# Optimization experiments

Hardware: AMD Instinct MI355X
Metric: run time of the kernel (lower is better)

Reference implementation:

```python
import jax, jax.numpy as jnp
import numpy as np

NS, NR, D, H, O = 50000, 100000, 128, 128, 2
ESR, ERR, ESS = 1000000, 1600000, 800000


def _sage(x_src, x_dst, src, dst, Wl, bl, Wr, num_dst):
    # PyG SAGEConv(aggr='mean'): lin_l(mean_{j in N(i)} x_j) + lin_r(x_i)
    s = jax.ops.segment_sum(x_src[src], dst, num_segments=num_dst)
    cnt = jax.ops.segment_sum(jnp.ones(dst.shape, x_src.dtype), dst, num_segments=num_dst)
    agg = s / jnp.maximum(cnt, 1.0)[:, None]
    return agg @ Wl + bl + x_dst @ Wr


def setup_inputs() -> dict:
    key = jax.random.key(0)
    ks = jax.random.split(key, 32)
    f = lambda i, shp: jax.random.normal(ks[i], shp, jnp.float32) * 0.05
    inp = {"x_subject": f(0, (NS, D)), "x_roi": f(1, (NR, D))}
    wnames = ["w1_sr_l", "w1_sr_r", "w1_rr_l", "w1_rr_r", "w1_ss_l", "w1_ss_r",
              "w2_sr_l", "w2_sr_r", "w2_rr_l", "w2_rr_r", "w2_ss_l", "w2_ss_r"]
    for i, n in enumerate(wnames):
        inp[n] = f(2 + i, (D if n[1] == '1' else H, H))
    for n in ["b1_sr", "b1_rr", "b1_ss", "b2_sr", "b2_rr", "b2_ss"]:
        inp[n] = jnp.zeros((H,), jnp.float32)
    inp["lin_w"] = f(14, (H, O))
    inp["lin_b"] = jnp.zeros((O,), jnp.float32)
    inp["ei_sr_src"] = jax.random.randint(ks[20], (ESR,), 0, NS, jnp.int32)
    inp["ei_sr_dst"] = jax.random.randint(ks[21], (ESR,), 0, NR, jnp.int32)
    inp["ei_rr_src"] = jax.random.randint(ks[22], (ERR,), 0, NR, jnp.int32)
    inp["ei_rr_dst"] = jax.random.randint(ks[23], (ERR,), 0, NR, jnp.int32)
    inp["ei_ss_src"] = jax.random.randint(ks[24], (ESS,), 0, NS, jnp.int32)
    inp["ei_ss_dst"] = jax.random.randint(ks[25], (ESS,), 0, NS, jnp.int32)
    return inp


def reference(x_subject, x_roi,
              w1_sr_l, b1_sr, w1_sr_r, w1_rr_l, b1_rr, w1_rr_r, w1_ss_l, b1_ss, w1_ss_r,
              w2_sr_l, b2_sr, w2_sr_r, w2_rr_l, b2_rr, w2_rr_r, w2_ss_l, b2_ss, w2_ss_r,
              lin_w, lin_b,
              ei_sr_src, ei_sr_dst, ei_rr_src, ei_rr_dst, ei_ss_src, ei_ss_dst):
    # layer 1: HeteroConv with aggr='mean' over per-edge-type outputs
    r1 = 0.5 * (_sage(x_subject, x_roi, ei_sr_src, ei_sr_dst, w1_sr_l, b1_sr, w1_sr_r, NR)
                + _sage(x_roi, x_roi, ei_rr_src, ei_rr_dst, w1_rr_l, b1_rr, w1_rr_r, NR))
    s1 = _sage(x_subject, x_subject, ei_ss_src, ei_ss_dst, w1_ss_l, b1_ss, w1_ss_r, NS)
    r1, s1 = jax.nn.relu(r1), jax.nn.relu(s1)
    # layer 2 (roi branch is dead code w.r.t. the output, which reads only 'subject')
    s2 = _sage(s1, s1, ei_ss_src, ei_ss_dst, w2_ss_l, b2_ss, w2_ss_r, NS)
    s2 = jax.nn.relu(s2)
    return s2 @ lin_w + lin_b
```

## Files before the change

### kernel.cpp

```cpp
#include <hip/hip_runtime.h>

#define NS   50000
#define ESS  800000
#define D    128

#define BSPAN 256
#define NB    ((NS + BSPAN - 1) / BSPAN)
#define EPB   4096
#define NBLK  ((ESS + EPB - 1) / EPB)
#define BCAP  8192

#define SPLIT_BLOCKS (NS * D / 8 / 256)
#define PREP_BLOCKS  256

typedef __attribute__((ext_vector_type(8))) short bf16x8;
typedef __attribute__((ext_vector_type(4))) float f32x4;

static __device__ __forceinline__ ushort f2bf(float f) {
    uint u = __float_as_uint(f);
    u += 0x7fffu + ((u >> 16) & 1u);
    return (ushort)(u >> 16);
}
static __device__ __forceinline__ float bf2f(ushort h) {
    return __uint_as_float((uint)h << 16);
}

__global__ __launch_bounds__(256) void splitprep_k(
    const float* __restrict__ x, ushort* __restrict__ xh,
    const float* __restrict__ w1l, const float* __restrict__ w1r,
    const float* __restrict__ w2l, const float* __restrict__ w2r,
    ushort* __restrict__ wt1h, ushort* __restrict__ wt1l,
    ushort* __restrict__ wt2h, ushort* __restrict__ wt2l,
    int* __restrict__ btotal)
{
    int blk = blockIdx.x, t = threadIdx.x;
    if (blk < SPLIT_BLOCKS) {
        int i = blk * 256 + t;
        const float4* src = (const float4*)(x + (size_t)i * 8);
        float4 a = src[0], b = src[1];
        uint4 o;
        o.x = (uint)f2bf(a.x) | ((uint)f2bf(a.y) << 16);
        o.y = (uint)f2bf(a.z) | ((uint)f2bf(a.w) << 16);
        o.z = (uint)f2bf(b.x) | ((uint)f2bf(b.y) << 16);
        o.w = (uint)f2bf(b.z) | ((uint)f2bf(b.w) << 16);
        *(uint4*)(xh + (size_t)i * 8) = o;
    } else if (blk < SPLIT_BLOCKS + PREP_BLOCKS) {
        int g = (blk - SPLIT_BLOCKS) * 256 + t;
        int layer = g >> 15;
        int rem   = g & 32767;
        int k     = rem >> 7;
        int col   = rem & 127;
        const float* wl = layer ? w2l : w1l;
        const float* wr = layer ? w2r : w1r;
        float v = (k < 128) ? wl[k * 128 + col] : wr[(k - 128) * 128 + col];
        ushort h = f2bf(v);
        ushort l = f2bf(v - bf2f(h));
        size_t idx = ((size_t)((k >> 5) * 4 + ((k >> 3) & 3)) * 128 + col) * 8 + (k & 7);
        (layer ? wt2h : wt1h)[idx] = h;
        (layer ? wt2l : wt1l)[idx] = l;
    } else {
        if (t < NB) btotal[t] = 0;
    }
}

__global__ __launch_bounds__(256) void pack_k(
    const int* __restrict__ src, const int* __restrict__ dst,
    uint* __restrict__ staging, int* __restrict__ blockhist,
    int* __restrict__ blockstart, int* __restrict__ btotal)
{
    __shared__ uint ldata[EPB];
    __shared__ int lh[256], lofs[256], lcur[256];
    int t = threadIdx.x, blk = blockIdx.x;
    int base = blk * EPB;
    int nmine = min(EPB, ESS - base);
    lh[t] = 0;
    __syncthreads();
    for (int i = t; i < nmine; i += 256) {
        int s = src[base + i], d = dst[base + i];
        ldata[i] = (uint)s | ((uint)(d & 255) << 16) | ((uint)(d >> 8) << 24);
        atomicAdd(&lh[d >> 8], 1);
    }
    __syncthreads();
    int v = lh[t];
    lofs[t] = v;
    __syncthreads();
    for (int off = 1; off < 256; off <<= 1) {
        int o = (t >= off) ? lofs[t - off] : 0;
        __syncthreads();
        lofs[t] += o;
        __syncthreads();
    }
    int excl = lofs[t] - v;
    if (t < NB) {
        blockhist[blk * NB + t]  = v;
        blockstart[blk * NB + t] = excl;
        if (v) atomicAdd(&btotal[t], v);
    }
    lcur[t] = excl;
    __syncthreads();
    for (int i = t; i < nmine; i += 256) {
        uint p = ldata[i];
        int slot = atomicAdd(&lcur[p >> 24], 1);
        staging[base + slot] = p;
    }
}

__global__ __launch_bounds__(256) void scan196_k(
    const int* __restrict__ btotal, int* __restrict__ bucket_base)
{
    __shared__ int lds[256];
    int t = threadIdx.x;
    int v = (t < NB) ? btotal[t] : 0;
    lds[t] = v;
    __syncthreads();
    for (int off = 1; off < 256; off <<= 1) {
        int o = (t >= off) ? lds[t - off] : 0;
        __syncthreads();
        lds[t] += o;
        __syncthreads();
    }
    if (t < NB) bucket_base[t] = lds[t] - v;
}

__global__ __launch_bounds__(256) void bucket_csr_k(
    const uint* __restrict__ staging, const int* __restrict__ blockhist,
    const int* __restrict__ blockstart, const int* __restrict__ bucket_base,
    int* __restrict__ deg, int* __restrict__ row_start, int* __restrict__ esrc)
{
    __shared__ uint bdata[BCAP];
    __shared__ int lscan[256], ldeg[256], lcur[256];
    int b = blockIdx.x, t = threadIdx.x;
    int c = (t < NBLK) ? blockhist[t * NB + b] : 0;
    lscan[t] = c;
    __syncthreads();
    for (int off = 1; off < 256; off <<= 1) {
        int o = (t >= off) ? lscan[t - off] : 0;
        __syncthreads();
        lscan[t] += o;
        __syncthreads();
    }
    int total = min(lscan[255], BCAP);
    int excl  = lscan[t] - c;
    if (t < NBLK && c > 0) {
        const uint* sp = staging + (size_t)t * EPB + blockstart[t * NB + b];
        for (int i = 0; i < c; ++i)
            if (excl + i < BCAP) bdata[excl + i] = sp[i];
    }
    ldeg[t] = 0;
    __syncthreads();
    for (int i = t; i < total; i += 256)
        atomicAdd(&ldeg[(bdata[i] >> 16) & 255], 1);
    __syncthreads();
    int v = ldeg[t];
    lscan[t] = v;
    __syncthreads();
    for (int off = 1; off < 256; off <<= 1) {
        int o = (t >= off) ? lscan[t - off] : 0;
        __syncthreads();
        lscan[t] += o;
        __syncthreads();
    }
    int nexcl = lscan[t] - v;
    int gbase = bucket_base[b];
    int node  = b * BSPAN + t;
    if (node < NS) {
        deg[node] = v;
        row_start[node] = gbase + nexcl;
    }
    lcur[t] = nexcl;
    __syncthreads();
    for (int i = t; i < total; i += 256) {
        uint p = bdata[i];
        int slot = atomicAdd(&lcur[(p >> 16) & 255], 1);
        esrc[gbase + slot] = (int)(p & 0xffffu);
    }
}

__global__ __launch_bounds__(256) void gather_mean_bf16_k(
    const ushort* __restrict__ xh, const int* __restrict__ esrc,
    const int* __restrict__ row_start, const int* __restrict__ deg,
    ushort* __restrict__ aggh, ushort* __restrict__ aggl, int M)
{
    int d = blockIdx.x * 4 + (threadIdx.x >> 6);
    if (d >= M) return;
    int lane = threadIdx.x & 63;
    int beg = row_start[d];
    int n   = deg[d];
    const uint* xp = reinterpret_cast<const uint*>(xh);
    float sx[8] = {}, sy[8] = {};
    for (int j = 0; j < n; j += 8) {
        uint u[8];
        bool m[8];
        #pragma unroll
        for (int q = 0; q < 8; ++q) {
            int jq = j + q;
            bool ok = jq < n;
            int s = esrc[beg + (ok ? jq : 0)];
            u[q] = xp[(size_t)s * 64 + lane];
            m[q] = ok;
        }
        #pragma unroll
        for (int q = 0; q < 8; ++q) {
            if (m[q]) {
                sx[q] += __uint_as_float(u[q] << 16);
                sy[q] += __uint_as_float(u[q] & 0xffff0000u);
            }
        }
    }
    float ax = ((sx[0] + sx[1]) + (sx[2] + sx[3])) + ((sx[4] + sx[5]) + (sx[6] + sx[7]));
    float ay = ((sy[0] + sy[1]) + (sy[2] + sy[3])) + ((sy[4] + sy[5]) + (sy[6] + sy[7]));
    float scale = 1.0f / fmaxf((float)n, 1.0f);
    ax *= scale; ay *= scale;
    ushort hx = f2bf(ax), hy = f2bf(ay);
    ushort lx = f2bf(ax - bf2f(hx)), ly = f2bf(ay - bf2f(hy));
    reinterpret_cast<uint*>(aggh)[(size_t)d * 64 + lane] = (uint)hx | ((uint)hy << 16);
    reinterpret_cast<uint*>(aggl)[(size_t)d * 64 + lane] = (uint)lx | ((uint)ly << 16);
}

template<bool FINAL>
__global__ __launch_bounds__(256) void sage_mfma_k(
    const ushort* __restrict__ aggh, const ushort* __restrict__ aggl,
    const ushort* __restrict__ xh,
    const ushort* __restrict__ wth, const ushort* __restrict__ wtl,
    const float* __restrict__ bias,
    ushort* __restrict__ s_out,
    const float* __restrict__ lin_w, const float* __restrict__ lin_b,
    float* __restrict__ out, int M)
{
    __shared__ __align__(16) ushort Ahs[8][4][64][8];
    __shared__ __align__(16) ushort Als[4][4][64][8];
    __shared__ float lps[2][32][2];

    const int t    = threadIdx.x;
    const int rb   = blockIdx.x * 64;
    const int wid  = t >> 6;
    const int wm   = wid >> 1;
    const int wn   = wid & 1;
    const int lane = t & 63;
    const int lr   = lane & 15;
    const int kg   = lane >> 4;

    {
        int row = t >> 2, q = t & 3;
        int grow = rb + row;
        bool ok = grow < M;
        #pragma unroll
        for (int i = 0; i < 8; ++i) {
            const ushort* sp = (i < 4)
                ? aggh + (size_t)grow * 128 + i * 32 + q * 8
                : xh   + (size_t)grow * 128 + (i - 4) * 32 + q * 8;
            uint4 v = make_uint4(0, 0, 0, 0);
            if (ok) v = *(const uint4*)sp;
            *(uint4*)&Ahs[i][q][row][0] = v;
        }
        #pragma unroll
        for (int i = 0; i < 4; ++i) {
            const ushort* sp = aggl + (size_t)grow * 128 + i * 32 + q * 8;
            uint4 v = make_uint4(0, 0, 0, 0);
            if (ok) v = *(const uint4*)sp;
            *(uint4*)&Als[i][q][row][0] = v;
        }
    }
    __syncthreads();

    f32x4 acc[2][4] = {};
    #pragma unroll
    for (int ks = 0; ks < 8; ++ks) {
        const bool isAgg = (ks < 4);
        bf16x8 ah[2], al[2], bh[4], bl[4];
        #pragma unroll
        for (int nt = 0; nt < 4; ++nt) {
            int c = wn * 64 + nt * 16 + lr;
            size_t off = ((size_t)(ks * 4 + kg) * 128 + c) * 8;
            bh[nt] = *(const bf16x8*)(wth + off);
            bl[nt] = *(const bf16x8*)(wtl + off);
        }
        #pragma unroll
        for (int mt = 0; mt < 2; ++mt) {
            int r = wm * 32 + mt * 16 + lr;
            ah[mt] = *(const bf16x8*)&Ahs[ks][kg][r][0];
            al[mt] = isAgg ? *(const bf16x8*)&Als[ks][kg][r][0] : ah[mt];
        }
        #pragma unroll
        for (int mt = 0; mt < 2; ++mt) {
            #pragma unroll
            for (int nt = 0; nt < 4; ++nt) {
                acc[mt][nt] = __builtin_amdgcn_mfma_f32_16x16x32_bf16(
                    ah[mt], bh[nt], acc[mt][nt], 0, 0, 0);
                acc[mt][nt] = __builtin_amdgcn_mfma_f32_16x16x32_bf16(
                    ah[mt], bl[nt], acc[mt][nt], 0, 0, 0);
                if (isAgg)
                    acc[mt][nt] = __builtin_amdgcn_mfma_f32_16x16x32_bf16(
                        al[mt], bh[nt], acc[mt][nt], 0, 0, 0);
            }
        }
    }

    if constexpr (FINAL) {
        float pv[2][4][2];
        #pragma unroll
        for (int mt = 0; mt < 2; ++mt) {
            #pragma unroll
            for (int r = 0; r < 4; ++r) {
                float p0 = 0.f, p1 = 0.f;
                #pragma unroll
                for (int nt = 0; nt < 4; ++nt) {
                    int col = wn * 64 + nt * 16 + lr;
                    float v = fmaxf(acc[mt][nt][r] + bias[col], 0.f);
                    float2 lw = *(const float2*)(lin_w + col * 2);
                    p0 += v * lw.x;
                    p1 += v * lw.y;
                }
                #pragma unroll
                for (int off = 1; off < 16; off <<= 1) {
                    p0 += __shfl_xor(p0, off);
                    p1 += __shfl_xor(p1, off);
                }
                pv[mt][r][0] = p0;
                pv[mt][r][1] = p1;
            }
        }
        if (wn == 1 && lr == 0) {
            #pragma unroll
            for (int mt = 0; mt < 2; ++mt)
                #pragma unroll
                for (int r = 0; r < 4; ++r) {
                    int row = mt * 16 + kg * 4 + r;
                    lps[wm][row][0] = pv[mt][r][0];
                    lps[wm][row][1] = pv[mt][r][1];
                }
        }
        __syncthreads();
        if (wn == 0 && lr == 0) {
            #pragma unroll
            for (int mt = 0; mt < 2; ++mt)
                #pragma unroll
                for (int r = 0; r < 4; ++r) {
                    int row = mt * 16 + kg * 4 + r;
                    int grow = rb + wm * 32 + row;
                    if (grow < M) {
                        out[(size_t)grow * 2 + 0] = pv[mt][r][0] + lps[wm][row][0] + lin_b[0];
                        out[(size_t)grow * 2 + 1] = pv[mt][r][1] + lps[wm][row][1] + lin_b[1];
                    }
                }
        }
    } else {
        #pragma unroll
        for (int mt = 0; mt < 2; ++mt) {
            #pragma unroll
            for (int r = 0; r < 4; ++r) {
                int grow = rb + wm * 32 + mt * 16 + kg * 4 + r;
                #pragma unroll
                for (int nt = 0; nt < 4; ++nt) {
                    int col = wn * 64 + nt * 16 + lr;
                    float v = fmaxf(acc[mt][nt][r] + bias[col], 0.f);
                    if (grow < M)
                        s_out[(size_t)grow * 128 + col] = f2bf(v);
                }
            }
        }
    }
}

extern "C" void kernel_launch(void* const* d_in, const int* in_sizes, int n_in,
                              void* d_out, int out_size, void* d_ws, size_t ws_size,
                              hipStream_t stream)
{
    const float* x_subject = (const float*)d_in[0];
    const float* w1l  = (const float*)d_in[6];
    const float* w1r  = (const float*)d_in[7];
    const float* w2l  = (const float*)d_in[12];
    const float* w2r  = (const float*)d_in[13];
    const float* b1   = (const float*)d_in[16];
    const float* b2   = (const float*)d_in[19];
    const float* linw = (const float*)d_in[20];
    const float* linb = (const float*)d_in[21];
    const int* ss_src = (const int*)d_in[26];
    const int* ss_dst = (const int*)d_in[27];

    char* wp = (char*)d_ws;
    ushort* xh        = (ushort*)wp; wp += (size_t)NS * D * 2;
    ushort* s1h       = (ushort*)wp; wp += (size_t)NS * D * 2;
    ushort* aggh      = (ushort*)wp; wp += (size_t)NS * D * 2;
    ushort* aggl      = (ushort*)wp; wp += (size_t)NS * D * 2;
    ushort* wt1h      = (ushort*)wp; wp += 256 * 128 * 2;
    ushort* wt1l      = (ushort*)wp; wp += 256 * 128 * 2;
    ushort* wt2h      = (ushort*)wp; wp += 256 * 128 * 2;
    ushort* wt2l      = (ushort*)wp; wp += 256 * 128 * 2;
    uint*  staging    = (uint*)wp;  wp += (size_t)NBLK * EPB * 4;
    int*   esrc       = (int*)wp;   wp += (size_t)ESS * 4;
    int*   blockhist  = (int*)wp;   wp += (size_t)NBLK * NB * 4;
    int*   blockstart = (int*)wp;   wp += (size_t)NBLK * NB * 4;
    int*   btotal     = (int*)wp;   wp += NB * 4;
    int*   bucket_base= (int*)wp;   wp += NB * 4;
    int*   deg        = (int*)wp;   wp += NS * 4;
    int*   row_start  = (int*)wp;   wp += NS * 4;

    const int gath_blocks = (NS + 3) / 4;
    const int gemm_blocks = (NS + 63) / 64;

    splitprep_k<<<SPLIT_BLOCKS + PREP_BLOCKS + 1, 256, 0, stream>>>(
        x_subject, xh, w1l, w1r, w2l, w2r, wt1h, wt1l, wt2h, wt2l, btotal);

    pack_k<<<NBLK, 256, 0, stream>>>(ss_src, ss_dst, staging,
                                     blockhist, blockstart, btotal);
    scan196_k<<<1, 256, 0, stream>>>(btotal, bucket_base);
    bucket_csr_k<<<NB, 256, 0, stream>>>(staging, blockhist, blockstart,
                                         bucket_base, deg, row_start, esrc);

    gather_mean_bf16_k<<<gath_blocks, 256, 0, stream>>>(xh, esrc, row_start,
                                                        deg, aggh, aggl, NS);
    sage_mfma_k<false><<<gemm_blocks, 256, 0, stream>>>(
        aggh, aggl, xh, wt1h, wt1l, b1, s1h, nullptr, nullptr, nullptr, NS);

    gather_mean_bf16_k<<<gath_blocks, 256, 0, stream>>>(s1h, esrc, row_start,
                                                        deg, aggh, aggl, NS);
    sage_mfma_k<true><<<gemm_blocks, 256, 0, stream>>>(
        aggh, aggl, s1h, wt2h, wt2l, b2, nullptr, linw, linb, (float*)d_out, NS);
}
```

Baseline: 311.1 us.

## Pad CSR rows to multiples of eight with a zero sentinel row, drop global scan

The CSR build now gives each bucket a fixed BCAP-sized region and pads every node's edge list to a multiple of 8 with a sentinel index pointing at an extra zero row appended to the feature buffers. This removes the btotal atomics and the separate single-block scan kernel, so one launch goes away. The gather loop loads its eight indices as two uint4 vector reads of byte offsets precomputed by the CSR pass, and drops the per-edge bounds masks. In exchange the padding adds wasted loads of the zero row, esrc grows to NB*BCAP entries, and rows are no longer packed contiguously.

```diff
diff --git a/kernel.cpp b/kernel.cpp
--- a/kernel.cpp
+++ b/kernel.cpp
@@ -27,11 +27,11 @@
 
 __global__ __launch_bounds__(256) void splitprep_k(
     const float* __restrict__ x, ushort* __restrict__ xh,
+    ushort* __restrict__ s1h,
     const float* __restrict__ w1l, const float* __restrict__ w1r,
     const float* __restrict__ w2l, const float* __restrict__ w2r,
     ushort* __restrict__ wt1h, ushort* __restrict__ wt1l,
-    ushort* __restrict__ wt2h, ushort* __restrict__ wt2l,
-    int* __restrict__ btotal)
+    ushort* __restrict__ wt2h, ushort* __restrict__ wt2l)
 {
     int blk = blockIdx.x, t = threadIdx.x;
     if (blk < SPLIT_BLOCKS) {
@@ -59,14 +59,15 @@
         (layer ? wt2h : wt1h)[idx] = h;
         (layer ? wt2l : wt1l)[idx] = l;
     } else {
-        if (t < NB) btotal[t] = 0;
+        if (t < 64)        ((uint*)(xh + (size_t)NS * D))[t] = 0u;
+        else if (t < 128)  ((uint*)(s1h + (size_t)NS * D))[t - 64] = 0u;
     }
 }
 
 __global__ __launch_bounds__(256) void pack_k(
     const int* __restrict__ src, const int* __restrict__ dst,
     uint* __restrict__ staging, int* __restrict__ blockhist,
-    int* __restrict__ blockstart, int* __restrict__ btotal)
+    int* __restrict__ blockstart)
 {
     __shared__ uint ldata[EPB];
     __shared__ int lh[256], lofs[256], lcur[256];
@@ -94,7 +95,6 @@
     if (t < NB) {
         blockhist[blk * NB + t]  = v;
         blockstart[blk * NB + t] = excl;
-        if (v) atomicAdd(&btotal[t], v);
     }
     lcur[t] = excl;
     __syncthreads();
@@ -105,27 +105,10 @@
     }
 }
 
-__global__ __launch_bounds__(256) void scan196_k(
-    const int* __restrict__ btotal, int* __restrict__ bucket_base)
-{
-    __shared__ int lds[256];
-    int t = threadIdx.x;
-    int v = (t < NB) ? btotal[t] : 0;
-    lds[t] = v;
-    __syncthreads();
-    for (int off = 1; off < 256; off <<= 1) {
-        int o = (t >= off) ? lds[t - off] : 0;
-        __syncthreads();
-        lds[t] += o;
-        __syncthreads();
-    }
-    if (t < NB) bucket_base[t] = lds[t] - v;
-}
-
 __global__ __launch_bounds__(256) void bucket_csr_k(
     const uint* __restrict__ staging, const int* __restrict__ blockhist,
-    const int* __restrict__ blockstart, const int* __restrict__ bucket_base,
-    int* __restrict__ deg, int* __restrict__ row_start, int* __restrict__ esrc)
+    const int* __restrict__ blockstart,
+    int* __restrict__ deg, int* __restrict__ row_start, uint* __restrict__ esrc)
 {
     __shared__ uint bdata[BCAP];
     __shared__ int lscan[256], ldeg[256], lcur[256];
@@ -151,8 +134,9 @@
     for (int i = t; i < total; i += 256)
         atomicAdd(&ldeg[(bdata[i] >> 16) & 255], 1);
     __syncthreads();
-    int v = ldeg[t];
-    lscan[t] = v;
+    int v  = ldeg[t];
+    int pv = (v + 7) & ~7;
+    lscan[t] = pv;
     __syncthreads();
     for (int off = 1; off < 256; off <<= 1) {
         int o = (t >= off) ? lscan[t - off] : 0;
@@ -160,24 +144,26 @@
         lscan[t] += o;
         __syncthreads();
     }
-    int nexcl = lscan[t] - v;
-    int gbase = bucket_base[b];
+    int pexcl = lscan[t] - pv;
+    int gbase = b * BCAP;
     int node  = b * BSPAN + t;
     if (node < NS) {
         deg[node] = v;
-        row_start[node] = gbase + nexcl;
-    }
-    lcur[t] = nexcl;
+        row_start[node] = gbase + pexcl;
+    }
+    lcur[t] = pexcl;
     __syncthreads();
     for (int i = t; i < total; i += 256) {
         uint p = bdata[i];
         int slot = atomicAdd(&lcur[(p >> 16) & 255], 1);
-        esrc[gbase + slot] = (int)(p & 0xffffu);
-    }
+        esrc[gbase + slot] = (p & 0xffffu) << 8;
+    }
+    for (int i = v; i < pv; ++i)
+        esrc[gbase + pexcl + i] = (uint)NS << 8;
 }
 
 __global__ __launch_bounds__(256) void gather_mean_bf16_k(
-    const ushort* __restrict__ xh, const int* __restrict__ esrc,
+    const ushort* __restrict__ xh, const uint* __restrict__ esrc,
     const int* __restrict__ row_start, const int* __restrict__ deg,
     ushort* __restrict__ aggh, ushort* __restrict__ aggl, int M)
 {
@@ -186,25 +172,27 @@
     int lane = threadIdx.x & 63;
     int beg = row_start[d];
     int n   = deg[d];
-    const uint* xp = reinterpret_cast<const uint*>(xh);
+    int pn8 = (n + 7) >> 3;
+    const char* base = (const char*)xh;
+    uint laneoff = (uint)lane << 2;
+    const uint4* ip = (const uint4*)(esrc + beg);
     float sx[8] = {}, sy[8] = {};
-    for (int j = 0; j < n; j += 8) {
+    for (int j = 0; j < pn8; ++j) {
+        uint4 o0 = ip[j * 2 + 0];
+        uint4 o1 = ip[j * 2 + 1];
         uint u[8];
-        bool m[8];
+        u[0] = *(const uint*)(base + (o0.x + laneoff));
+        u[1] = *(const uint*)(base + (o0.y + laneoff));
+        u[2] = *(const uint*)(base + (o0.z + laneoff));
+        u[3] = *(const uint*)(base + (o0.w + laneoff));
+        u[4] = *(const uint*)(base + (o1.x + laneoff));
+        u[5] = *(const uint*)(base + (o1.y + laneoff));
+        u[6] = *(const uint*)(base + (o1.z + laneoff));
+        u[7] = *(const uint*)(base + (o1.w + laneoff));
         #pragma unroll
         for (int q = 0; q < 8; ++q) {
-            int jq = j + q;
-            bool ok = jq < n;
-            int s = esrc[beg + (ok ? jq : 0)];
-            u[q] = xp[(size_t)s * 64 + lane];
-            m[q] = ok;
-        }
-        #pragma unroll
-        for (int q = 0; q < 8; ++q) {
-            if (m[q]) {
-                sx[q] += __uint_as_float(u[q] << 16);
-                sy[q] += __uint_as_float(u[q] & 0xffff0000u);
-            }
+            sx[q] += __uint_as_float(u[q] << 16);
+            sy[q] += __uint_as_float(u[q] & 0xffff0000u);
         }
     }
     float ax = ((sx[0] + sx[1]) + (sx[2] + sx[3])) + ((sx[4] + sx[5]) + (sx[6] + sx[7]));
@@ -379,8 +367,8 @@
     const int* ss_dst = (const int*)d_in[27];
 
     char* wp = (char*)d_ws;
-    ushort* xh        = (ushort*)wp; wp += (size_t)NS * D * 2;
-    ushort* s1h       = (ushort*)wp; wp += (size_t)NS * D * 2;
+    ushort* xh        = (ushort*)wp; wp += (size_t)(NS + 1) * D * 2;
+    ushort* s1h       = (ushort*)wp; wp += (size_t)(NS + 1) * D * 2;
     ushort* aggh      = (ushort*)wp; wp += (size_t)NS * D * 2;
     ushort* aggl      = (ushort*)wp; wp += (size_t)NS * D * 2;
     ushort* wt1h      = (ushort*)wp; wp += 256 * 128 * 2;
@@ -388,11 +376,9 @@
     ushort* wt2h      = (ushort*)wp; wp += 256 * 128 * 2;
     ushort* wt2l      = (ushort*)wp; wp += 256 * 128 * 2;
     uint*  staging    = (uint*)wp;  wp += (size_t)NBLK * EPB * 4;
-    int*   esrc       = (int*)wp;   wp += (size_t)ESS * 4;
+    uint*  esrc       = (uint*)wp;  wp += (size_t)NB * BCAP * 4;
     int*   blockhist  = (int*)wp;   wp += (size_t)NBLK * NB * 4;
     int*   blockstart = (int*)wp;   wp += (size_t)NBLK * NB * 4;
-    int*   btotal     = (int*)wp;   wp += NB * 4;
-    int*   bucket_base= (int*)wp;   wp += NB * 4;
     int*   deg        = (int*)wp;   wp += NS * 4;
     int*   row_start  = (int*)wp;   wp += NS * 4;
 
@@ -400,13 +386,12 @@
     const int gemm_blocks = (NS + 63) / 64;
 
     splitprep_k<<<SPLIT_BLOCKS + PREP_BLOCKS + 1, 256, 0, stream>>>(
-        x_subject, xh, w1l, w1r, w2l, w2r, wt1h, wt1l, wt2h, wt2l, btotal);
+        x_subject, xh, s1h, w1l, w1r, w2l, w2r, wt1h, wt1l, wt2h, wt2l);
 
     pack_k<<<NBLK, 256, 0, stream>>>(ss_src, ss_dst, staging,
-                                     blockhist, blockstart, btotal);
-    scan196_k<<<1, 256, 0, stream>>>(btotal, bucket_base);
+                                     blockhist, blockstart);
     bucket_csr_k<<<NB, 256, 0, stream>>>(staging, blockhist, blockstart,
-                                         bucket_base, deg, row_start, esrc);
+                                         deg, row_start, esrc);
 
     gather_mean_bf16_k<<<gath_blocks, 256, 0, stream>>>(xh, esrc, row_start,
                                                         deg, aggh, aggl, NS);
```

New measurement: 293.3 us. 5.7% less time.
